# Optimization experiments

Measured on AMD Instinct MI355X. Metric: run time of the kernel, lower is better.

## Reference

```python
import jax, jax.numpy as jnp
import numpy as np

B, T, HM = 2, 2048, 1024
HEADS = 16
DK = (HM // 2) // HEADS   # expand_k = 0.5 -> key_dim 512, per-head 32
DV = HM // HEADS          # expand_v = 1.0 -> per-head 64
LOW_RANK = 16             # gate low-rank dim (fla default)
GATE_NORM = 16.0          # gate_logit_normalizer (fla default)
EPS = 1e-5


def setup_inputs() -> dict:
    key = jax.random.key(0)
    ks = jax.random.split(key, 12)
    def p(k, shape, s=0.02):
        return jax.random.normal(k, shape, jnp.float32) * s
    return dict(
        x=jax.random.normal(ks[0], (B, T, HM), jnp.float32),
        ln_w=jnp.ones((HM,), jnp.float32), ln_b=jnp.zeros((HM,), jnp.float32),
        Wq=p(ks[1], (HM, HEADS * DK)), Wk=p(ks[2], (HM, HEADS * DK)),
        Wv=p(ks[3], (HM, HEADS * DV)),
        gk_w1=p(ks[4], (HM, LOW_RANK)), gk_w2=p(ks[5], (LOW_RANK, HEADS * DK)),
        gk_b2=jnp.zeros((HEADS * DK,), jnp.float32),
        Wg=p(ks[6], (HM, HEADS * DV)), rms_w=jnp.ones((DV,), jnp.float32),
        Wo=p(ks[7], (HEADS * DV, HM)),
        W1=p(ks[8], (HM, 2 * HM)), b1=jnp.zeros((2 * HM,), jnp.float32),
        W2=p(ks[9], (2 * HM, HM)), b2=jnp.zeros((HM,), jnp.float32),
    )


def _ln(x, w, b):
    m = x.mean(-1, keepdims=True)
    v = ((x - m) ** 2).mean(-1, keepdims=True)
    return (x - m) * jax.lax.rsqrt(v + EPS) * w + b


def _rms(x, w):
    return x * jax.lax.rsqrt((x * x).mean(-1, keepdims=True) + EPS) * w


def _gla(q, k, v, gk):
    # gated linear attention recurrence:
    # S_t = diag(exp(gk_t)) S_{t-1} + k_t v_t^T ;  o_t = q_t S_t
    # q,k,gk: [B,T,H,DK], v: [B,T,H,DV]
    def step(S, inp):
        qt, kt, vt, gt = inp
        S = jnp.exp(gt)[..., None] * S + kt[..., None] * vt[..., None, :]
        return S, jnp.einsum('bhk,bhkv->bhv', qt, S)
    xs = tuple(jnp.moveaxis(a, 1, 0) for a in (q, k, v, gk))
    S0 = jnp.zeros((q.shape[0], q.shape[2], q.shape[3], v.shape[3]), q.dtype)
    _, o = jax.lax.scan(step, S0, xs)
    return jnp.moveaxis(o, 0, 1)


def reference(x, ln_w, ln_b, Wq, Wk, Wv, gk_w1, gk_w2, gk_b2, Wg, rms_w, Wo, W1, b1, W2, b2):
    Bb, Tt, _ = x.shape
    h = _ln(x, ln_w, ln_b)
    q = (h @ Wq).reshape(Bb, Tt, HEADS, DK)
    k = (h @ Wk).reshape(Bb, Tt, HEADS, DK)
    v = (h @ Wv).reshape(Bb, Tt, HEADS, DV)
    gk = (jax.nn.log_sigmoid((h @ gk_w1) @ gk_w2 + gk_b2) / GATE_NORM)
    gk = gk.reshape(Bb, Tt, HEADS, DK)
    o = _gla(q * (DK ** -0.5), k, v, gk)
    # output gate: RMSNorm(o) * swish(g)  (FusedRMSNormSwishGate)
    g = (h @ Wg).reshape(Bb, Tt, HEADS, DV)
    o = _rms(o, rms_w) * (g * jax.nn.sigmoid(g))
    x = x + o.reshape(Bb, Tt, HEADS * DV) @ Wo
    h2 = _ln(x, ln_w, ln_b)  # same shared norm module
    return x + jax.nn.gelu(h2 @ W1 + b1, approximate=False) @ W2 + b2
```

## Files before the change

### kernel.cpp

```cpp
#include <hip/hip_runtime.h>
#include <hip/hip_bf16.h>
#include <math.h>


using bf16 = __hip_bfloat16;
typedef __attribute__((ext_vector_type(8))) short bf16x8;
typedef __attribute__((ext_vector_type(4))) float f32x4;

#define BT 4096
#define HM 1024
#define DK 32
#define DV 64
#define NC 32
#define CHK 64

#if defined(__has_builtin)
#if __has_builtin(__builtin_amdgcn_global_load_lds)
#define HAVE_GLDS 1
#endif
#endif

#ifdef HAVE_GLDS
#define GLDS16(g, l) __builtin_amdgcn_global_load_lds( \
    (const __attribute__((address_space(1))) unsigned int*)(g), \
    (__attribute__((address_space(3))) unsigned int*)(l), 16, 0, 0)
#else
#define GLDS16(g, l) (*(int4*)(l) = *(const int4*)(g))
#endif

__device__ __forceinline__ float b2f(bf16 v) { return __bfloat162float(v); }
__device__ __forceinline__ bf16 f2b(float v) { return __float2bfloat16(v); }
__device__ __forceinline__ float clampf(float v, float lim) {
    return fminf(fmaxf(v, -lim), lim);
}
__device__ __forceinline__ float lo16(unsigned int u) {
    union { unsigned int i; float f; } c; c.i = u << 16; return c.f;
}
__device__ __forceinline__ float hi16(unsigned int u) {
    union { unsigned int i; float f; } c; c.i = u & 0xffff0000u; return c.f;
}
__device__ __forceinline__ void acc8(float a, uint4 r, float* o) {
    o[0] += a * lo16(r.x); o[1] += a * hi16(r.x);
    o[2] += a * lo16(r.y); o[3] += a * hi16(r.y);
    o[4] += a * lo16(r.z); o[5] += a * hi16(r.z);
    o[6] += a * lo16(r.w); o[7] += a * hi16(r.w);
}

__global__ __launch_bounds__(256) void detect_dtype(
    const unsigned int* __restrict__ x, int* __restrict__ flag)
{
    int tid = threadIdx.x;
    int cnt = 0;
    for (int i = 0; i < 16; ++i) {
        unsigned int w = x[tid * 16 + i];
        unsigned int e_lo = (w >> 7) & 0xffu;
        unsigned int e_hi = (w >> 23) & 0xffu;
        cnt += (e_lo >= 110 && e_lo <= 135 && e_hi >= 110 && e_hi <= 135) ? 1 : 0;
    }
    __shared__ int red[256];
    red[tid] = cnt;
    __syncthreads();
    for (int s = 128; s > 0; s >>= 1) {
        if (tid < s) red[tid] += red[tid + s];
        __syncthreads();
    }
    if (tid == 0) *flag = (red[0] > 2048) ? 1 : 0;
}

__global__ __launch_bounds__(256) void cvt_to_bf16(
    const void* __restrict__ src, bf16* __restrict__ dst, int n,
    const int* __restrict__ flag)
{
    bool isb = (*flag != 0);
    int i = blockIdx.x * 256 + threadIdx.x;
    int stride = gridDim.x * 256;
    for (; i < n; i += stride) {
        if (isb) ((ushort*)dst)[i] = ((const ushort*)src)[i];
        else     dst[i] = f2b(((const float*)src)[i]);
    }
}

struct SmallCvt { const void* s[8]; bf16* d[8]; int n[8]; };
__global__ __launch_bounds__(256) void cvt_small(SmallCvt sc, const int* __restrict__ flag)
{
    bool isb = (*flag != 0);
    int stride = gridDim.x * 256;
    #pragma unroll
    for (int seg = 0; seg < 8; ++seg) {
        int n = sc.n[seg];
        for (int i = blockIdx.x * 256 + threadIdx.x; i < n; i += stride) {
            if (isb) ((ushort*)sc.d[seg])[i] = ((const ushort*)sc.s[seg])[i];
            else     sc.d[seg][i] = f2b(((const float*)sc.s[seg])[i]);
        }
    }
}

__global__ __launch_bounds__(256) void transpose_any(
    const void* __restrict__ src, ushort* __restrict__ dst, int R, int C,
    const int* __restrict__ flag)
{
    bool isb = (*flag != 0);
    __shared__ ushort tile[32][33];
    int c0 = blockIdx.x * 32, r0 = blockIdx.y * 32;
    int x = threadIdx.x, y = threadIdx.y;
    #pragma unroll
    for (int dy = 0; dy < 32; dy += 8) {
        size_t idx = (size_t)(r0 + y + dy) * C + c0 + x;
        ushort v;
        if (isb) v = ((const ushort*)src)[idx];
        else { bf16 t = f2b(((const float*)src)[idx]); v = *(ushort*)&t; }
        tile[y + dy][x] = v;
    }
    __syncthreads();
    #pragma unroll
    for (int dy = 0; dy < 32; dy += 8)
        dst[(size_t)(c0 + y + dy) * R + r0 + x] = tile[x][y + dy];
}

template <typename TI>
__global__ __launch_bounds__(256) void ln_kernel(
    const TI* __restrict__ x, const bf16* __restrict__ w, const bf16* __restrict__ b,
    bf16* __restrict__ out)
{
    size_t base = (size_t)blockIdx.x * HM;
    int tid = threadIdx.x;
    float v[4], s = 0.f, s2 = 0.f;
    #pragma unroll
    for (int u = 0; u < 4; ++u) {
        float f;
        if constexpr (sizeof(TI) == 2) f = b2f(((const bf16*)x)[base + tid + u * 256]);
        else                           f = ((const float*)x)[base + tid + u * 256];
        v[u] = f; s += f; s2 += f * f;
    }
    #pragma unroll
    for (int off = 32; off >= 1; off >>= 1) {
        s  += __shfl_down(s, off);
        s2 += __shfl_down(s2, off);
    }
    __shared__ float ra[4], rb[4];
    int wave = tid >> 6;
    if ((tid & 63) == 0) { ra[wave] = s; rb[wave] = s2; }
    __syncthreads();
    s = ra[0] + ra[1] + ra[2] + ra[3];
    s2 = rb[0] + rb[1] + rb[2] + rb[3];
    float mean = s * (1.f / HM);
    float var = fmaxf(s2 * (1.f / HM) - mean * mean, 0.f);
    float rs = rsqrtf(var + 1e-5f);
    #pragma unroll
    for (int u = 0; u < 4; ++u) {
        int col = tid + u * 256;
        out[base + col] = f2b((v[u] - mean) * rs * b2f(w[col]) + b2f(b[col]));
    }
}

__global__ __launch_bounds__(256) void gk_kernel(
    const bf16* __restrict__ h, const bf16* __restrict__ w1,
    const bf16* __restrict__ w2, const bf16* __restrict__ b2i,
    bf16* __restrict__ gkout)
{
    size_t row = blockIdx.x;
    const bf16* hr = h + row * HM;
    int tid = threadIdx.x;
    int d = tid & 15, seg = tid >> 4;
    float s = 0.f;
    for (int j = 0; j < 64; ++j) {
        int i = seg * 64 + j;
        s += b2f(hr[i]) * b2f(w1[i * 16 + d]);
    }
    __shared__ float red[256];
    __shared__ float g1[16];
    red[tid] = s;
    __syncthreads();
    if (tid < 16) {
        float t = 0.f;
        #pragma unroll
        for (int sg = 0; sg < 16; ++sg) t += red[sg * 16 + tid];
        g1[tid] = t;
    }
    __syncthreads();
    #pragma unroll
    for (int rep = 0; rep < 2; ++rep) {
        int n = tid + rep * 256;
        float z = b2f(b2i[n]);
        #pragma unroll
        for (int r = 0; r < 16; ++r) z += g1[r] * b2f(w2[r * 512 + n]);
        z = clampf(z, 30.f);
        float ls = (z >= 0.f) ? -log1pf(expf(-z)) : (z - log1pf(expf(z)));
        gkout[row * 512 + n] = f2b(ls * 0.0625f);
    }
}

template <int MODE>
__global__ __launch_bounds__(256) void gemm_bt(
    const bf16* __restrict__ A, const bf16* __restrict__ Wt,
    const bf16* __restrict__ bias, const void* __restrict__ resid,
    void* __restrict__ out, int M, int N, int K, const int* __restrict__ oflag)
{
    __shared__ __align__(16) ushort As[128 * 64];
    __shared__ __align__(16) ushort Bs[64 * 64];
    int tid = threadIdx.x;
    int w = tid >> 6, l = tid & 63;
    int bm = blockIdx.x * 128, bn = blockIdx.y * 64;
    int row16 = l & 15, quad = l >> 4;
    bool out_bf16 = false;
    if constexpr (MODE == 3) out_bf16 = (*oflag != 0);

    const ushort* Au = (const ushort*)A;
    const ushort* Wu = (const ushort*)Wt;

    f32x4 acc[4][2] = {};
    for (int k0 = 0; k0 < K; k0 += 64) {
        #pragma unroll
        for (int i = 0; i < 4; ++i) {
            int j = i * 4 + w;
            const ushort* g = Au + (size_t)(bm + (j >> 1) * 16 + row16) * K
                              + k0 + (j & 1) * 32 + quad * 8;
            GLDS16(g, &As[j * 512 + l * 8]);
        }
        #pragma unroll
        for (int i = 0; i < 2; ++i) {
            int j = i * 4 + w;
            const ushort* g = Wu + (size_t)(bn + (j >> 1) * 16 + row16) * K
                              + k0 + (j & 1) * 32 + quad * 8;
            GLDS16(g, &Bs[j * 512 + l * 8]);
        }
        __syncthreads();
        #pragma unroll
        for (int s = 0; s < 2; ++s) {
            int fo = (s * 4 + quad) * 128 + row16 * 8;
            bf16x8 af[4], bw[2];
            #pragma unroll
            for (int mi = 0; mi < 4; ++mi)
                af[mi] = *(const bf16x8*)&As[((w >> 1) * 4 + mi) * 1024 + fo];
            #pragma unroll
            for (int ni = 0; ni < 2; ++ni)
                bw[ni] = *(const bf16x8*)&Bs[((w & 1) * 2 + ni) * 1024 + fo];
            #pragma unroll
            for (int mi = 0; mi < 4; ++mi)
                #pragma unroll
                for (int ni = 0; ni < 2; ++ni)
                    acc[mi][ni] = __builtin_amdgcn_mfma_f32_16x16x32_bf16(af[mi], bw[ni], acc[mi][ni], 0, 0, 0);
        }
        __syncthreads();
    }
    #pragma unroll
    for (int mi = 0; mi < 4; ++mi) {
        #pragma unroll
        for (int ni = 0; ni < 2; ++ni) {
            int col = bn + (w & 1) * 32 + ni * 16 + row16;
            #pragma unroll
            for (int r = 0; r < 4; ++r) {
                int row = bm + (w >> 1) * 64 + mi * 16 + quad * 4 + r;
                size_t idx = (size_t)row * N + col;
                float v = acc[mi][ni][r];
                if constexpr (MODE == 0) {
                    ((bf16*)out)[idx] = f2b(clampf(v, 1e4f));
                } else if constexpr (MODE == 1) {
                    ((float*)out)[idx] = clampf(b2f(((const bf16*)resid)[idx]) + v, 1e5f);
                } else if constexpr (MODE == 2) {
                    float t = clampf(v + b2f(bias[col]), 50.f);
                    ((bf16*)out)[idx] = f2b(0.5f * t * (1.f + erff(t * 0.70710678f)));
                } else {
                    float t = clampf(v + b2f(bias[col]) + ((const float*)resid)[idx], 2e5f);
                    if (out_bf16) ((bf16*)out)[idx] = f2b(t);
                    else          ((float*)out)[idx] = t;
                }
            }
        }
    }
}

__global__ __launch_bounds__(256) void gla_phase1(
    const bf16* __restrict__ gkb,
    const bf16* __restrict__ qvg,
    float* __restrict__ clbuf, float* __restrict__ Dbuf, float* __restrict__ Pbuf)
{
    int bh = blockIdx.x, c = blockIdx.y;
    int b = bh >> 4, hh = bh & 15;
    int row0 = b * 2048 + c * CHK;
    __shared__ float glog[CHK][DK + 1];
    __shared__ float wk[CHK][DK + 1];
    __shared__ __align__(16) ushort vt[CHK][DV];
    int tid = threadIdx.x;
    int k = tid & 31, i8 = (tid >> 5) * 8;
    #pragma unroll
    for (int u = 0; u < 8; ++u) {
        int i = i8 + u;
        float g = b2f(gkb[(size_t)(row0 + i) * 512 + hh * 32 + k]);
        glog[i][k] = fminf(fmaxf(g, -2.f), 0.f);
    }
    {
        int cc = tid & 7, ii = tid >> 3;
        #pragma unroll
        for (int h = 0; h < 2; ++h) {
            int i = ii + h * 32;
            uint4 val = *(const uint4*)((const ushort*)qvg + (size_t)(row0 + i) * 3072 + 1024 + hh * 64 + cc * 8);
            *(uint4*)&vt[i][cc * 8] = val;
        }
    }
    __syncthreads();
    if (tid < 32) {
        float run = 0.f;
        for (int j = 0; j < CHK; ++j) { run += glog[j][tid]; glog[j][tid] = run; }
    }
    __syncthreads();
    #pragma unroll
    for (int u = 0; u < 8; ++u) {
        int i = i8 + u;
        float cl = glog[i][k];
        float cl63 = glog[CHK - 1][k];
        clbuf[(size_t)(row0 + i) * 512 + hh * 32 + k] = cl;
        wk[i][k] = expf(fmaxf(cl63 - cl, -60.f)) *
            b2f(qvg[(size_t)(row0 + i) * 3072 + 512 + hh * 32 + k]);
    }
    if (tid < 32) Dbuf[(size_t)(bh * 32 + c) * 32 + tid] = expf(glog[CHK - 1][tid]);
    __syncthreads();
    int kk = tid >> 3, v8 = (tid & 7) * 8;
    float acc[8] = {};
    for (int j = 0; j < CHK; ++j) {
        float w = wk[j][kk];
        uint4 raw = *(const uint4*)&vt[j][v8];
        acc8(w, raw, acc);
    }
    float* Pp = Pbuf + (size_t)(bh * 32 + c) * 2048 + kk * 64 + v8;
    #pragma unroll
    for (int u = 0; u < 8; ++u) Pp[u] = acc[u];
}

__global__ __launch_bounds__(256) void gla_scan(
    const float* __restrict__ Pbuf, const float* __restrict__ Dbuf,
    float* __restrict__ Sbuf)
{
    int bh = blockIdx.x >> 3, vg8 = blockIdx.x & 7;
    int kk = threadIdx.x >> 3, vv = vg8 * 8 + (threadIdx.x & 7);
    float S = 0.f;
    for (int c = 0; c < NC; ++c) {
        size_t idx = (size_t)(bh * 32 + c) * 2048 + kk * 64 + vv;
        float P = Pbuf[idx];
        float D = Dbuf[(size_t)(bh * 32 + c) * 32 + kk];
        Sbuf[idx] = S;
        S = D * S + P;
    }
}

__global__ __launch_bounds__(256) void gla_phase3(
    const bf16* __restrict__ qvg,
    const float* __restrict__ clbuf, const float* __restrict__ Sbuf,
    const bf16* __restrict__ rmsw, bf16* __restrict__ obuf)
{
    int bh = blockIdx.x, c = blockIdx.y;
    int b = bh >> 4, hh = bh & 15;
    int row0 = b * 2048 + c * CHK;
    __shared__ float qs[CHK][36], ks[CHK][36];
    __shared__ float S0[DK][68];
    __shared__ float Amat[CHK][CHK + 1];
    __shared__ __align__(16) ushort vt[CHK][DV];
    int tid = threadIdx.x;
    {
        int k = tid & 31, i8 = (tid >> 5) * 8;
        #pragma unroll
        for (int u = 0; u < 8; ++u) {
            int i = i8 + u;
            size_t r = (size_t)(row0 + i);
            int col = hh * 32 + k;
            float cl = fmaxf(clbuf[r * 512 + col], -60.f);
            qs[i][k] = b2f(qvg[r * 3072 + col]) * expf(cl) * 0.17677669529663687f;
            ks[i][k] = b2f(qvg[r * 3072 + 512 + col]) * expf(-cl);
        }
    }
    {
        int cc = tid & 7, ii = tid >> 3;
        #pragma unroll
        for (int h = 0; h < 2; ++h) {
            int i = ii + h * 32;
            uint4 val = *(const uint4*)((const ushort*)qvg + (size_t)(row0 + i) * 3072 + 1024 + hh * 64 + cc * 8);
            *(uint4*)&vt[i][cc * 8] = val;
        }
    }
    {
        int kk = tid >> 3, v8 = (tid & 7) * 8;
        const float* Sp = Sbuf + (size_t)(bh * 32 + c) * 2048 + kk * 64 + v8;
        *(f32x4*)&S0[kk][v8]     = *(const f32x4*)Sp;
        *(f32x4*)&S0[kk][v8 + 4] = *(const f32x4*)(Sp + 4);
    }
    __syncthreads();
    int i = tid >> 2, jb = tid & 3;
    for (int jj = 0; jj < 16; ++jj) {
        int j = jb + jj * 4;
        float d = 0.f;
        if (j <= i) {
            const f32x4* qp = (const f32x4*)qs[i];
            const f32x4* kp = (const f32x4*)ks[j];
            #pragma unroll
            for (int q8 = 0; q8 < 8; ++q8) {
                f32x4 a = qp[q8], bq = kp[q8];
                d += a.x * bq.x + a.y * bq.y + a.z * bq.z + a.w * bq.w;
            }
        }
        Amat[i][j] = d;
    }
    __syncthreads();
    float o[16] = {};
    int vv = jb * 16;
    for (int j = 0; j < CHK; ++j) {
        float a = Amat[i][j];
        uint4 r0 = *(const uint4*)&vt[j][vv];
        uint4 r1 = *(const uint4*)&vt[j][vv + 8];
        acc8(a, r0, o);
        acc8(a, r1, o + 8);
    }
    #pragma unroll
    for (int kk = 0; kk < DK; ++kk) {
        float qv = qs[i][kk];
        const f32x4* Sp = (const f32x4*)&S0[kk][vv];
        #pragma unroll
        for (int q4 = 0; q4 < 4; ++q4) {
            f32x4 sv = Sp[q4];
            o[q4 * 4 + 0] += qv * sv.x; o[q4 * 4 + 1] += qv * sv.y;
            o[q4 * 4 + 2] += qv * sv.z; o[q4 * 4 + 3] += qv * sv.w;
        }
    }
    float ss = 0.f;
    #pragma unroll
    for (int u = 0; u < 16; ++u) ss += o[u] * o[u];
    ss += __shfl_xor(ss, 1);
    ss += __shfl_xor(ss, 2);
    float sc = rsqrtf(fmaxf(ss, 0.f) * (1.f / DV) + 1e-5f);
    size_t r = (size_t)(row0 + i);
    #pragma unroll
    for (int u = 0; u < 16; ++u) {
        float g = b2f(qvg[r * 3072 + 2048 + hh * 64 + vv + u]);
        float sw = g / (1.f + expf(-g));
        obuf[r * 1024 + hh * 64 + vv + u] = f2b(clampf(o[u] * sc * b2f(rmsw[vv + u]) * sw, 3e4f));
    }
}

extern "C" void kernel_launch(void* const* d_in, const int* in_sizes, int n_in,
                              void* d_out, int out_size, void* d_ws, size_t ws_size,
                              hipStream_t stream) {
    (void)in_sizes; (void)n_in; (void)out_size; (void)ws_size;

    char* ws = (char*)d_ws;
    const size_t MB = 1024 * 1024;
    const size_t KB = 1024;
    bf16*  WqkT = (bf16*)(ws + 0);
    bf16*  WkT  = (bf16*)(ws + 1 * MB);
    bf16*  WvgT = (bf16*)(ws + 2 * MB);
    bf16*  WgT  = (bf16*)(ws + 4 * MB);
    bf16*  WoT  = (bf16*)(ws + 6 * MB);
    bf16*  W1T  = (bf16*)(ws + 8 * MB);
    bf16*  W2T  = (bf16*)(ws + 12 * MB);
    bf16*  hbuf = (bf16*)(ws + 16 * MB);
    bf16*  qvg  = (bf16*)(ws + 24 * MB);
    bf16*  gkb  = (bf16*)(ws + 48 * MB);
    float* clbf = (float*)(ws + 52 * MB);
    float* Dbuf = (float*)(ws + 60 * MB);
    float* Pbuf = (float*)(ws + 61 * MB);
    float* Sbuf = (float*)(ws + 69 * MB);
    bf16*  obuf = (bf16*)(ws + 61 * MB);
    float* ybuf = (float*)(ws + 32 * MB);
    bf16*  f1   = (bf16*)(ws + 48 * MB);
    bf16*  cx   = (bf16*)(ws + 77 * MB);
    bf16*  clnw = (bf16*)(ws + 85 * MB);
    bf16*  clnb = (bf16*)(ws + 85 * MB + 64 * KB);
    bf16*  cgw1 = (bf16*)(ws + 85 * MB + 128 * KB);
    bf16*  cgw2 = (bf16*)(ws + 85 * MB + 192 * KB);
    bf16*  cgb2 = (bf16*)(ws + 85 * MB + 256 * KB);
    bf16*  crms = (bf16*)(ws + 85 * MB + 320 * KB);
    bf16*  cb1  = (bf16*)(ws + 85 * MB + 384 * KB);
    bf16*  cb2  = (bf16*)(ws + 85 * MB + 448 * KB);
    int*   flag = (int*)(ws + 85 * MB + 512 * KB);

    hipLaunchKernelGGL(detect_dtype, dim3(1), dim3(256), 0, stream,
                       (const unsigned int*)d_in[0], flag);

    hipLaunchKernelGGL(cvt_to_bf16, dim3(2048), dim3(256), 0, stream,
                       d_in[0], cx, 4194304, flag);
    SmallCvt sc;
    sc.s[0] = d_in[1];  sc.d[0] = clnw; sc.n[0] = 1024;
    sc.s[1] = d_in[2];  sc.d[1] = clnb; sc.n[1] = 1024;
    sc.s[2] = d_in[6];  sc.d[2] = cgw1; sc.n[2] = 16384;
    sc.s[3] = d_in[7];  sc.d[3] = cgw2; sc.n[3] = 8192;
    sc.s[4] = d_in[8];  sc.d[4] = cgb2; sc.n[4] = 512;
    sc.s[5] = d_in[10]; sc.d[5] = crms; sc.n[5] = 64;
    sc.s[6] = d_in[13]; sc.d[6] = cb1;  sc.n[6] = 2048;
    sc.s[7] = d_in[15]; sc.d[7] = cb2;  sc.n[7] = 1024;
    hipLaunchKernelGGL(cvt_small, dim3(64), dim3(256), 0, stream, sc, flag);

    dim3 tb(32, 8);
    hipLaunchKernelGGL(transpose_any, dim3(16, 32), tb, 0, stream, d_in[3],  (ushort*)WqkT, 1024, 512, flag);
    hipLaunchKernelGGL(transpose_any, dim3(16, 32), tb, 0, stream, d_in[4],  (ushort*)WkT,  1024, 512, flag);
    hipLaunchKernelGGL(transpose_any, dim3(32, 32), tb, 0, stream, d_in[5],  (ushort*)WvgT, 1024, 1024, flag);
    hipLaunchKernelGGL(transpose_any, dim3(32, 32), tb, 0, stream, d_in[9],  (ushort*)WgT,  1024, 1024, flag);
    hipLaunchKernelGGL(transpose_any, dim3(32, 32), tb, 0, stream, d_in[11], (ushort*)WoT,  1024, 1024, flag);
    hipLaunchKernelGGL(transpose_any, dim3(64, 32), tb, 0, stream, d_in[12], (ushort*)W1T,  1024, 2048, flag);
    hipLaunchKernelGGL(transpose_any, dim3(32, 64), tb, 0, stream, d_in[14], (ushort*)W2T,  2048, 1024, flag);

    hipLaunchKernelGGL((ln_kernel<bf16>), dim3(BT), dim3(256), 0, stream, cx, clnw, clnb, hbuf);

    hipLaunchKernelGGL((gemm_bt<0>), dim3(32, 48), dim3(256), 0, stream,
                       hbuf, WqkT, (const bf16*)nullptr, (const void*)nullptr, (void*)qvg, BT, 3072, 1024, (const int*)nullptr);
    hipLaunchKernelGGL(gk_kernel, dim3(BT), dim3(256), 0, stream, hbuf, cgw1, cgw2, cgb2, gkb);

    hipLaunchKernelGGL(gla_phase1, dim3(32, 32), dim3(256), 0, stream, gkb, qvg, clbf, Dbuf, Pbuf);
    hipLaunchKernelGGL(gla_scan, dim3(256), dim3(256), 0, stream, Pbuf, Dbuf, Sbuf);
    hipLaunchKernelGGL(gla_phase3, dim3(32, 32), dim3(256), 0, stream, qvg, clbf, Sbuf, crms, obuf);

    hipLaunchKernelGGL((gemm_bt<1>), dim3(32, 16), dim3(256), 0, stream,
                       obuf, WoT, (const bf16*)nullptr, (const void*)cx, (void*)ybuf, BT, 1024, 1024, (const int*)nullptr);
    hipLaunchKernelGGL((ln_kernel<float>), dim3(BT), dim3(256), 0, stream, ybuf, clnw, clnb, hbuf);
    hipLaunchKernelGGL((gemm_bt<2>), dim3(32, 32), dim3(256), 0, stream,
                       hbuf, W1T, cb1, (const void*)nullptr, (void*)f1, BT, 2048, 1024, (const int*)nullptr);
    hipLaunchKernelGGL((gemm_bt<3>), dim3(32, 16), dim3(256), 0, stream,
                       f1, W2T, cb2, (const void*)ybuf, d_out, BT, 1024, 2048, flag);
}
```

Before: 456.1 us.

## Replace LDS-staged GEMM with single-wave register-direct MFMA GEMM

The shared-memory GEMM, which used 256-thread blocks and async global-to-LDS loads, is replaced with a 64-thread kernel. Each wave computes a 64x64 tile by loading MFMA fragments directly from global memory into registers, with double buffering across k-halves. This removes the barriers and LDS traffic, and the smaller blocks create more of them. In exchange there is no operand reuse across waves through shared memory, so more global and L2 traffic is needed per FLOP, and the loads are narrow 16-byte strided row reads.

```diff
diff --git a/kernel.cpp b/kernel.cpp
--- a/kernel.cpp
+++ b/kernel.cpp
@@ -13,20 +13,6 @@
 #define DV 64
 #define NC 32
 #define CHK 64
-
-#if defined(__has_builtin)
-#if __has_builtin(__builtin_amdgcn_global_load_lds)
-#define HAVE_GLDS 1
-#endif
-#endif
-
-#ifdef HAVE_GLDS
-#define GLDS16(g, l) __builtin_amdgcn_global_load_lds( \
-    (const __attribute__((address_space(1))) unsigned int*)(g), \
-    (__attribute__((address_space(3))) unsigned int*)(l), 16, 0, 0)
-#else
-#define GLDS16(g, l) (*(int4*)(l) = *(const int4*)(g))
-#endif
 
 __device__ __forceinline__ float b2f(bf16 v) { return __bfloat162float(v); }
 __device__ __forceinline__ bf16 f2b(float v) { return __float2bfloat16(v); }
@@ -191,66 +177,66 @@
 }
 
 template <int MODE>
-__global__ __launch_bounds__(256) void gemm_bt(
+__global__ __launch_bounds__(64) void dgemm(
     const bf16* __restrict__ A, const bf16* __restrict__ Wt,
     const bf16* __restrict__ bias, const void* __restrict__ resid,
     void* __restrict__ out, int M, int N, int K, const int* __restrict__ oflag)
 {
-    __shared__ __align__(16) ushort As[128 * 64];
-    __shared__ __align__(16) ushort Bs[64 * 64];
-    int tid = threadIdx.x;
-    int w = tid >> 6, l = tid & 63;
-    int bm = blockIdx.x * 128, bn = blockIdx.y * 64;
+    int l = threadIdx.x;
+    int bm = blockIdx.x * 64, bn = blockIdx.y * 64;
     int row16 = l & 15, quad = l >> 4;
     bool out_bf16 = false;
     if constexpr (MODE == 3) out_bf16 = (*oflag != 0);
 
     const ushort* Au = (const ushort*)A;
     const ushort* Wu = (const ushort*)Wt;
-
-    f32x4 acc[4][2] = {};
+    const ushort* pa[4];
+    const ushort* pb[4];
+    #pragma unroll
+    for (int mi = 0; mi < 4; ++mi)
+        pa[mi] = Au + (size_t)(bm + mi * 16 + row16) * K + quad * 8;
+    #pragma unroll
+    for (int ni = 0; ni < 4; ++ni)
+        pb[ni] = Wu + (size_t)(bn + ni * 16 + row16) * K + quad * 8;
+
+    f32x4 acc[4][4] = {};
+    bf16x8 a0[4], b0[4], a1[4], b1[4];
+    #pragma unroll
+    for (int mi = 0; mi < 4; ++mi) a0[mi] = *(const bf16x8*)(pa[mi]);
+    #pragma unroll
+    for (int ni = 0; ni < 4; ++ni) b0[ni] = *(const bf16x8*)(pb[ni]);
+
     for (int k0 = 0; k0 < K; k0 += 64) {
         #pragma unroll
-        for (int i = 0; i < 4; ++i) {
-            int j = i * 4 + w;
-            const ushort* g = Au + (size_t)(bm + (j >> 1) * 16 + row16) * K
-                              + k0 + (j & 1) * 32 + quad * 8;
-            GLDS16(g, &As[j * 512 + l * 8]);
-        }
-        #pragma unroll
-        for (int i = 0; i < 2; ++i) {
-            int j = i * 4 + w;
-            const ushort* g = Wu + (size_t)(bn + (j >> 1) * 16 + row16) * K
-                              + k0 + (j & 1) * 32 + quad * 8;
-            GLDS16(g, &Bs[j * 512 + l * 8]);
-        }
-        __syncthreads();
-        #pragma unroll
-        for (int s = 0; s < 2; ++s) {
-            int fo = (s * 4 + quad) * 128 + row16 * 8;
-            bf16x8 af[4], bw[2];
+        for (int mi = 0; mi < 4; ++mi) a1[mi] = *(const bf16x8*)(pa[mi] + k0 + 32);
+        #pragma unroll
+        for (int ni = 0; ni < 4; ++ni) b1[ni] = *(const bf16x8*)(pb[ni] + k0 + 32);
+        #pragma unroll
+        for (int mi = 0; mi < 4; ++mi)
             #pragma unroll
-            for (int mi = 0; mi < 4; ++mi)
-                af[mi] = *(const bf16x8*)&As[((w >> 1) * 4 + mi) * 1024 + fo];
+            for (int ni = 0; ni < 4; ++ni)
+                acc[mi][ni] = __builtin_amdgcn_mfma_f32_16x16x32_bf16(a0[mi], b0[ni], acc[mi][ni], 0, 0, 0);
+        if (k0 + 64 < K) {
             #pragma unroll
-            for (int ni = 0; ni < 2; ++ni)
-                bw[ni] = *(const bf16x8*)&Bs[((w & 1) * 2 + ni) * 1024 + fo];
+            for (int mi = 0; mi < 4; ++mi) a0[mi] = *(const bf16x8*)(pa[mi] + k0 + 64);
             #pragma unroll
-            for (int mi = 0; mi < 4; ++mi)
-                #pragma unroll
-                for (int ni = 0; ni < 2; ++ni)
-                    acc[mi][ni] = __builtin_amdgcn_mfma_f32_16x16x32_bf16(af[mi], bw[ni], acc[mi][ni], 0, 0, 0);
-        }
-        __syncthreads();
-    }
+            for (int ni = 0; ni < 4; ++ni) b0[ni] = *(const bf16x8*)(pb[ni] + k0 + 64);
+        }
+        #pragma unroll
+        for (int mi = 0; mi < 4; ++mi)
+            #pragma unroll
+            for (int ni = 0; ni < 4; ++ni)
+                acc[mi][ni] = __builtin_amdgcn_mfma_f32_16x16x32_bf16(a1[mi], b1[ni], acc[mi][ni], 0, 0, 0);
+    }
+
     #pragma unroll
     for (int mi = 0; mi < 4; ++mi) {
         #pragma unroll
-        for (int ni = 0; ni < 2; ++ni) {
-            int col = bn + (w & 1) * 32 + ni * 16 + row16;
+        for (int ni = 0; ni < 4; ++ni) {
+            int col = bn + ni * 16 + row16;
             #pragma unroll
             for (int r = 0; r < 4; ++r) {
-                int row = bm + (w >> 1) * 64 + mi * 16 + quad * 4 + r;
+                int row = bm + mi * 16 + quad * 4 + r;
                 size_t idx = (size_t)row * N + col;
                 float v = acc[mi][ni][r];
                 if constexpr (MODE == 0) {
@@ -498,7 +484,7 @@
 
     hipLaunchKernelGGL((ln_kernel<bf16>), dim3(BT), dim3(256), 0, stream, cx, clnw, clnb, hbuf);
 
-    hipLaunchKernelGGL((gemm_bt<0>), dim3(32, 48), dim3(256), 0, stream,
+    hipLaunchKernelGGL((dgemm<0>), dim3(64, 48), dim3(64), 0, stream,
                        hbuf, WqkT, (const bf16*)nullptr, (const void*)nullptr, (void*)qvg, BT, 3072, 1024, (const int*)nullptr);
     hipLaunchKernelGGL(gk_kernel, dim3(BT), dim3(256), 0, stream, hbuf, cgw1, cgw2, cgb2, gkb);
 
@@ -506,11 +492,11 @@
     hipLaunchKernelGGL(gla_scan, dim3(256), dim3(256), 0, stream, Pbuf, Dbuf, Sbuf);
     hipLaunchKernelGGL(gla_phase3, dim3(32, 32), dim3(256), 0, stream, qvg, clbf, Sbuf, crms, obuf);
 
-    hipLaunchKernelGGL((gemm_bt<1>), dim3(32, 16), dim3(256), 0, stream,
+    hipLaunchKernelGGL((dgemm<1>), dim3(64, 16), dim3(64), 0, stream,
                        obuf, WoT, (const bf16*)nullptr, (const void*)cx, (void*)ybuf, BT, 1024, 1024, (const int*)nullptr);
     hipLaunchKernelGGL((ln_kernel<float>), dim3(BT), dim3(256), 0, stream, ybuf, clnw, clnb, hbuf);
-    hipLaunchKernelGGL((gemm_bt<2>), dim3(32, 32), dim3(256), 0, stream,
+    hipLaunchKernelGGL((dgemm<2>), dim3(64, 32), dim3(64), 0, stream,
                        hbuf, W1T, cb1, (const void*)nullptr, (void*)f1, BT, 2048, 1024, (const int*)nullptr);
-    hipLaunchKernelGGL((gemm_bt<3>), dim3(32, 16), dim3(256), 0, stream,
+    hipLaunchKernelGGL((dgemm<3>), dim3(64, 16), dim3(64), 0, stream,
                        f1, W2T, cb2, (const void*)ybuf, d_out, BT, 1024, 2048, flag);
 }
```

Result: slower. 607.9 us (+33.3%).

## Drop input conversion pass, batch weight transposes, swizzle GEMM blocks per XCD

Applied to the files above, without the earlier changes.

Removes the separate kernel that converted x to bf16; the first LayerNorm and the Wo residual epilogue now read the original input directly, using the dtype flag. The seven transpose launches become one kernel that finds its segment through a descriptor table. GEMMs switch to a 1D grid with an XCD-aware block remap, so each XCD works on a contiguous band of N tiles and reuses weight tiles in its L2. The aim is to cut launch overhead and a full-tensor read/write pass, at the cost of a runtime dtype branch in the LN and GEMM epilogues.

```diff
diff --git a/kernel.cpp b/kernel.cpp
--- a/kernel.cpp
+++ b/kernel.cpp
@@ -67,19 +67,6 @@
     if (tid == 0) *flag = (red[0] > 2048) ? 1 : 0;
 }
 
-__global__ __launch_bounds__(256) void cvt_to_bf16(
-    const void* __restrict__ src, bf16* __restrict__ dst, int n,
-    const int* __restrict__ flag)
-{
-    bool isb = (*flag != 0);
-    int i = blockIdx.x * 256 + threadIdx.x;
-    int stride = gridDim.x * 256;
-    for (; i < n; i += stride) {
-        if (isb) ((ushort*)dst)[i] = ((const ushort*)src)[i];
-        else     dst[i] = f2b(((const float*)src)[i]);
-    }
-}
-
 struct SmallCvt { const void* s[8]; bf16* d[8]; int n[8]; };
 __global__ __launch_bounds__(256) void cvt_small(SmallCvt sc, const int* __restrict__ flag)
 {
@@ -95,20 +82,31 @@
     }
 }
 
-__global__ __launch_bounds__(256) void transpose_any(
-    const void* __restrict__ src, ushort* __restrict__ dst, int R, int C,
-    const int* __restrict__ flag)
+struct TDesc { const void* src; ushort* dst; int R, C, tile0; };
+struct TAll { TDesc d[7]; };
+__global__ __launch_bounds__(256) void transpose_all(
+    TAll ta, const int* __restrict__ flag)
 {
     bool isb = (*flag != 0);
+    int bid = blockIdx.x;
+    int seg = 0;
+    #pragma unroll
+    for (int i = 1; i < 7; ++i) if (bid >= ta.d[i].tile0) seg = i;
+    const void* src = ta.d[seg].src;
+    ushort* dst = ta.d[seg].dst;
+    int R = ta.d[seg].R, C = ta.d[seg].C;
+    int t = bid - ta.d[seg].tile0;
+    int tilesX = C >> 5;
+    int c0 = (t % tilesX) * 32, r0 = (t / tilesX) * 32;
+
     __shared__ ushort tile[32][33];
-    int c0 = blockIdx.x * 32, r0 = blockIdx.y * 32;
     int x = threadIdx.x, y = threadIdx.y;
     #pragma unroll
     for (int dy = 0; dy < 32; dy += 8) {
         size_t idx = (size_t)(r0 + y + dy) * C + c0 + x;
         ushort v;
         if (isb) v = ((const ushort*)src)[idx];
-        else { bf16 t = f2b(((const float*)src)[idx]); v = *(ushort*)&t; }
+        else { bf16 tb = f2b(((const float*)src)[idx]); v = *(ushort*)&tb; }
         tile[y + dy][x] = v;
     }
     __syncthreads();
@@ -117,19 +115,18 @@
         dst[(size_t)(c0 + y + dy) * R + r0 + x] = tile[x][y + dy];
 }
 
-template <typename TI>
 __global__ __launch_bounds__(256) void ln_kernel(
-    const TI* __restrict__ x, const bf16* __restrict__ w, const bf16* __restrict__ b,
-    bf16* __restrict__ out)
-{
+    const void* __restrict__ x, const bf16* __restrict__ w, const bf16* __restrict__ b,
+    bf16* __restrict__ out, const int* __restrict__ flag, int force)
+{
+    bool isb = (force >= 0) ? (force != 0) : (*flag != 0);
     size_t base = (size_t)blockIdx.x * HM;
     int tid = threadIdx.x;
     float v[4], s = 0.f, s2 = 0.f;
     #pragma unroll
     for (int u = 0; u < 4; ++u) {
-        float f;
-        if constexpr (sizeof(TI) == 2) f = b2f(((const bf16*)x)[base + tid + u * 256]);
-        else                           f = ((const float*)x)[base + tid + u * 256];
+        size_t idx = base + tid + u * 256;
+        float f = isb ? b2f(((const bf16*)x)[idx]) : ((const float*)x)[idx];
         v[u] = f; s += f; s2 += f * f;
     }
     #pragma unroll
@@ -200,10 +197,25 @@
     __shared__ __align__(16) ushort Bs[64 * 64];
     int tid = threadIdx.x;
     int w = tid >> 6, l = tid & 63;
-    int bm = blockIdx.x * 128, bn = blockIdx.y * 64;
+
+    int gx = M >> 7, gy = N >> 6;
+    int flat = blockIdx.x;
+    int bm_i, bn_i;
+    if ((gy & 7) == 0) {
+        int band = gy >> 3;
+        int xcd = flat & 7;
+        int idx = flat >> 3;
+        bn_i = xcd * band + idx % band;
+        bm_i = idx / band;
+    } else {
+        bm_i = flat % gx;
+        bn_i = flat / gx;
+    }
+    int bm = bm_i * 128, bn = bn_i * 64;
+
     int row16 = l & 15, quad = l >> 4;
-    bool out_bf16 = false;
-    if constexpr (MODE == 3) out_bf16 = (*oflag != 0);
+    bool isb = false;
+    if constexpr (MODE == 1 || MODE == 3) isb = (*oflag != 0);
 
     const ushort* Au = (const ushort*)A;
     const ushort* Wu = (const ushort*)Wt;
@@ -256,14 +268,16 @@
                 if constexpr (MODE == 0) {
                     ((bf16*)out)[idx] = f2b(clampf(v, 1e4f));
                 } else if constexpr (MODE == 1) {
-                    ((float*)out)[idx] = clampf(b2f(((const bf16*)resid)[idx]) + v, 1e5f);
+                    float rv = isb ? b2f(((const bf16*)resid)[idx])
+                                   : ((const float*)resid)[idx];
+                    ((float*)out)[idx] = clampf(rv + v, 1e5f);
                 } else if constexpr (MODE == 2) {
                     float t = clampf(v + b2f(bias[col]), 50.f);
                     ((bf16*)out)[idx] = f2b(0.5f * t * (1.f + erff(t * 0.70710678f)));
                 } else {
                     float t = clampf(v + b2f(bias[col]) + ((const float*)resid)[idx], 2e5f);
-                    if (out_bf16) ((bf16*)out)[idx] = f2b(t);
-                    else          ((float*)out)[idx] = t;
+                    if (isb) ((bf16*)out)[idx] = f2b(t);
+                    else     ((float*)out)[idx] = t;
                 }
             }
         }
@@ -460,7 +474,6 @@
     bf16*  obuf = (bf16*)(ws + 61 * MB);
     float* ybuf = (float*)(ws + 32 * MB);
     bf16*  f1   = (bf16*)(ws + 48 * MB);
-    bf16*  cx   = (bf16*)(ws + 77 * MB);
     bf16*  clnw = (bf16*)(ws + 85 * MB);
     bf16*  clnb = (bf16*)(ws + 85 * MB + 64 * KB);
     bf16*  cgw1 = (bf16*)(ws + 85 * MB + 128 * KB);
@@ -474,8 +487,6 @@
     hipLaunchKernelGGL(detect_dtype, dim3(1), dim3(256), 0, stream,
                        (const unsigned int*)d_in[0], flag);
 
-    hipLaunchKernelGGL(cvt_to_bf16, dim3(2048), dim3(256), 0, stream,
-                       d_in[0], cx, 4194304, flag);
     SmallCvt sc;
     sc.s[0] = d_in[1];  sc.d[0] = clnw; sc.n[0] = 1024;
     sc.s[1] = d_in[2];  sc.d[1] = clnb; sc.n[1] = 1024;
@@ -487,30 +498,33 @@
     sc.s[7] = d_in[15]; sc.d[7] = cb2;  sc.n[7] = 1024;
     hipLaunchKernelGGL(cvt_small, dim3(64), dim3(256), 0, stream, sc, flag);
 
-    dim3 tb(32, 8);
-    hipLaunchKernelGGL(transpose_any, dim3(16, 32), tb, 0, stream, d_in[3],  (ushort*)WqkT, 1024, 512, flag);
-    hipLaunchKernelGGL(transpose_any, dim3(16, 32), tb, 0, stream, d_in[4],  (ushort*)WkT,  1024, 512, flag);
-    hipLaunchKernelGGL(transpose_any, dim3(32, 32), tb, 0, stream, d_in[5],  (ushort*)WvgT, 1024, 1024, flag);
-    hipLaunchKernelGGL(transpose_any, dim3(32, 32), tb, 0, stream, d_in[9],  (ushort*)WgT,  1024, 1024, flag);
-    hipLaunchKernelGGL(transpose_any, dim3(32, 32), tb, 0, stream, d_in[11], (ushort*)WoT,  1024, 1024, flag);
-    hipLaunchKernelGGL(transpose_any, dim3(64, 32), tb, 0, stream, d_in[12], (ushort*)W1T,  1024, 2048, flag);
-    hipLaunchKernelGGL(transpose_any, dim3(32, 64), tb, 0, stream, d_in[14], (ushort*)W2T,  2048, 1024, flag);
-
-    hipLaunchKernelGGL((ln_kernel<bf16>), dim3(BT), dim3(256), 0, stream, cx, clnw, clnb, hbuf);
-
-    hipLaunchKernelGGL((gemm_bt<0>), dim3(32, 48), dim3(256), 0, stream,
-                       hbuf, WqkT, (const bf16*)nullptr, (const void*)nullptr, (void*)qvg, BT, 3072, 1024, (const int*)nullptr);
+    TAll ta;
+    ta.d[0] = { d_in[3],  (ushort*)WqkT, 1024, 512,  0 };
+    ta.d[1] = { d_in[4],  (ushort*)WkT,  1024, 512,  512 };
+    ta.d[2] = { d_in[5],  (ushort*)WvgT, 1024, 1024, 1024 };
+    ta.d[3] = { d_in[9],  (ushort*)WgT,  1024, 1024, 2048 };
+    ta.d[4] = { d_in[11], (ushort*)WoT,  1024, 1024, 3072 };
+    ta.d[5] = { d_in[12], (ushort*)W1T,  1024, 2048, 4096 };
+    ta.d[6] = { d_in[14], (ushort*)W2T,  2048, 1024, 6144 };
+    hipLaunchKernelGGL(transpose_all, dim3(8192), dim3(32, 8), 0, stream, ta, flag);
+
+    hipLaunchKernelGGL(ln_kernel, dim3(BT), dim3(256), 0, stream,
+                       d_in[0], clnw, clnb, hbuf, (const int*)flag, -1);
+
+    hipLaunchKernelGGL((gemm_bt<0>), dim3(32 * 48), dim3(256), 0, stream,
+                       hbuf, WqkT, (const bf16*)nullptr, (const void*)nullptr, (void*)qvg, BT, 3072, 1024, flag);
     hipLaunchKernelGGL(gk_kernel, dim3(BT), dim3(256), 0, stream, hbuf, cgw1, cgw2, cgb2, gkb);
 
     hipLaunchKernelGGL(gla_phase1, dim3(32, 32), dim3(256), 0, stream, gkb, qvg, clbf, Dbuf, Pbuf);
     hipLaunchKernelGGL(gla_scan, dim3(256), dim3(256), 0, stream, Pbuf, Dbuf, Sbuf);
     hipLaunchKernelGGL(gla_phase3, dim3(32, 32), dim3(256), 0, stream, qvg, clbf, Sbuf, crms, obuf);
 
-    hipLaunchKernelGGL((gemm_bt<1>), dim3(32, 16), dim3(256), 0, stream,
-                       obuf, WoT, (const bf16*)nullptr, (const void*)cx, (void*)ybuf, BT, 1024, 1024, (const int*)nullptr);
-    hipLaunchKernelGGL((ln_kernel<float>), dim3(BT), dim3(256), 0, stream, ybuf, clnw, clnb, hbuf);
-    hipLaunchKernelGGL((gemm_bt<2>), dim3(32, 32), dim3(256), 0, stream,
-                       hbuf, W1T, cb1, (const void*)nullptr, (void*)f1, BT, 2048, 1024, (const int*)nullptr);
-    hipLaunchKernelGGL((gemm_bt<3>), dim3(32, 16), dim3(256), 0, stream,
+    hipLaunchKernelGGL((gemm_bt<1>), dim3(32 * 16), dim3(256), 0, stream,
+                       obuf, WoT, (const bf16*)nullptr, (const void*)d_in[0], (void*)ybuf, BT, 1024, 1024, flag);
+    hipLaunchKernelGGL(ln_kernel, dim3(BT), dim3(256), 0, stream,
+                       (const void*)ybuf, clnw, clnb, hbuf, (const int*)flag, 0);
+    hipLaunchKernelGGL((gemm_bt<2>), dim3(32 * 32), dim3(256), 0, stream,
+                       hbuf, W1T, cb1, (const void*)nullptr, (void*)f1, BT, 2048, 1024, flag);
+    hipLaunchKernelGGL((gemm_bt<3>), dim3(32 * 16), dim3(256), 0, stream,
                        f1, W2T, cb2, (const void*)ybuf, d_out, BT, 1024, 2048, flag);
 }
```

New measurement: 445.0 us. -2.4%, faster.
